# Kernel tuning notes

Hardware: AMD Instinct MI355X
Metric: run time of the kernel (lower is better)

## Reference

```python
import jax, jax.numpy as jnp
import numpy as np

C = 512
NUM_HEADS = 8
GROUPS = 32
EPS = 1e-5
SHAPE = (1, C, 4, 32, 32)  # B, C, T, H, W


def setup_inputs() -> dict:
    key = jax.random.key(0)
    k_x, k_qkv, k_proj = jax.random.split(key, 3)
    # Small init scale on weights keeps softmax logits in a sane range.
    return {
        "x": jax.random.normal(k_x, SHAPE, dtype=jnp.float32),
        "gn_w": jnp.ones((C,), dtype=jnp.float32),
        "gn_b": jnp.zeros((C,), dtype=jnp.float32),
        "qkv_w": jax.random.normal(k_qkv, (3 * C, C), dtype=jnp.float32) * 0.02,
        "qkv_b": jnp.zeros((3 * C,), dtype=jnp.float32),
        "proj_w": jax.random.normal(k_proj, (C, C), dtype=jnp.float32) * 0.02,
        "proj_b": jnp.zeros((C,), dtype=jnp.float32),
    }


def reference(x, gn_w, gn_b, qkv_w, qkv_b, proj_w, proj_b):
    B, Cc, T, H, W = x.shape
    N = T * H * W
    nh = NUM_HEADS
    hd = Cc // nh

    # GroupNorm(32, C)
    xg = x.reshape(B, GROUPS, -1)
    mean = jnp.mean(xg, axis=-1, keepdims=True)
    var = jnp.var(xg, axis=-1, keepdims=True)
    xn = ((xg - mean) * jax.lax.rsqrt(var + EPS)).reshape(B, Cc, N)
    xn = xn * gn_w[None, :, None] + gn_b[None, :, None]

    # 1x1x1 conv == channel GEMM
    qkv = jnp.einsum('oc,bcn->bon', qkv_w, xn) + qkv_b[None, :, None]
    qkv = qkv.reshape(B, 3, nh, hd, N)
    q, k, v = qkv[:, 0], qkv[:, 1], qkv[:, 2]  # [B, nh, hd, N]

    scale = hd ** (-0.5)
    attn = jnp.einsum('bhdt,bhds->bhts', q, k) * scale  # [B, nh, N, N]
    attn = jax.nn.softmax(attn, axis=-1)
    out = jnp.einsum('bhts,bhds->bhdt', attn, v)  # [B, nh, hd, N]
    out = out.reshape(B, Cc, N)

    out = jnp.einsum('oc,bcn->bon', proj_w, out) + proj_b[None, :, None]
    return out.reshape(B, Cc, T, H, W) + x
```

## Files before the change

### kernel.cpp

```cpp
#include <hip/hip_runtime.h>
#include <hip/hip_bf16.h>

#define SEQN 4096
#define HD 64
#define CCH 512
#define NH 8
#define SC 4
#define CHUNK (SEQN / SC)

typedef __attribute__((ext_vector_type(8))) short short8;
typedef __attribute__((ext_vector_type(4))) float f32x4;

#define AS1 __attribute__((address_space(1)))
#define AS3 __attribute__((address_space(3)))

#if __has_builtin(__builtin_amdgcn_exp2f)
#define EXP2(x) __builtin_amdgcn_exp2f(x)
#else
#define EXP2(x) exp2f(x)
#endif

#define QSCALE 0.18033688011112042f

static __device__ __forceinline__ unsigned short f2bf(float f) {
    __hip_bfloat16 h = __float2bfloat16(f);
    return *(unsigned short*)&h;
}
static __device__ __forceinline__ float bf2f(unsigned short u) {
    unsigned int v = ((unsigned int)u) << 16;
    return *(float*)&v;
}
static __device__ __forceinline__ unsigned int fbits(float f) { return *(unsigned int*)&f; }
static __device__ __forceinline__ float hi_f(unsigned int v) {
    unsigned int t = v & 0xFFFF0000u; return *(float*)&t;
}
static __device__ __forceinline__ float lo_f(unsigned int v) {
    unsigned int t = v << 16; return *(float*)&t;
}
static __device__ __forceinline__ unsigned int pkbf(float lo, float hi) {
    return (fbits(hi) & 0xFFFF0000u) | (fbits(lo) >> 16);
}
static __device__ __forceinline__ short8 half_frag(unsigned int a, unsigned int b) {
    uint4 u; u.x = a; u.y = b; u.z = 0u; u.w = 0u;
    return __builtin_bit_cast(short8, u);
}
static __device__ __forceinline__ void load_lds_16(const unsigned short* g, unsigned short* l) {
    __builtin_amdgcn_global_load_lds((const AS1 void*)g, (AS3 void*)l, 16, 0, 0);
}

__global__ __launch_bounds__(256) void gn_stats(const float* __restrict__ x,
                                                float2* __restrict__ partials) {
    const int b = blockIdx.x;
    const int g = b >> 3;
    const int slice = b & 7;
    const float* xs = x + (size_t)g * 65536 + slice * 8192;
    const int tid = threadIdx.x;
    float s = 0.f, ss = 0.f;
    for (int i = tid; i < 2048; i += 256) {
        float4 v = ((const float4*)xs)[i];
        s  += v.x + v.y + v.z + v.w;
        ss += v.x * v.x + v.y * v.y + v.z * v.z + v.w * v.w;
    }
    for (int off = 32; off; off >>= 1) {
        s  += __shfl_xor(s, off);
        ss += __shfl_xor(ss, off);
    }
    __shared__ float red[8];
    const int wave = tid >> 6;
    const int lane = tid & 63;
    if (lane == 0) { red[wave] = s; red[4 + wave] = ss; }
    __syncthreads();
    if (tid == 0) {
        partials[b] = make_float2(red[0] + red[1] + red[2] + red[3],
                                  red[4] + red[5] + red[6] + red[7]);
    }
}

__global__ __launch_bounds__(256) void gn_norm_t(const float* __restrict__ x,
                                                 const float2* __restrict__ partials,
                                                 const float* __restrict__ w,
                                                 const float* __restrict__ b,
                                                 unsigned short* __restrict__ xnT) {
    __shared__ float tile[64][65];
    __shared__ float gmean[4], grstd[4];
    const int t0 = blockIdx.x * 64;
    const int c0 = blockIdx.y * 64;
    const int tid = threadIdx.x;
    if (tid < 4) {
        int g = (c0 >> 4) + tid;
        float s = 0.f, ss = 0.f;
#pragma unroll
        for (int i = 0; i < 8; i++) {
            float2 p = partials[g * 8 + i];
            s += p.x; ss += p.y;
        }
        float mean = s * (1.f / 65536.f);
        float var  = ss * (1.f / 65536.f) - mean * mean;
        gmean[tid] = mean;
        grstd[tid] = rsqrtf(var + 1e-5f);
    }
    __syncthreads();
    for (int e = tid; e < 1024; e += 256) {
        int r  = e >> 4;
        int t4 = (e & 15) << 2;
        int c = c0 + r;
        float rstd = grstd[r >> 4];
        float sc = w[c] * rstd;
        float sh = b[c] - gmean[r >> 4] * sc;
        float4 v = *(const float4*)(x + (size_t)c * SEQN + t0 + t4);
        tile[r][t4 + 0] = v.x * sc + sh;
        tile[r][t4 + 1] = v.y * sc + sh;
        tile[r][t4 + 2] = v.z * sc + sh;
        tile[r][t4 + 3] = v.w * sc + sh;
    }
    __syncthreads();
    for (int e = tid; e < 1024; e += 256) {
        int t  = e >> 4;
        int c4 = (e & 15) << 2;
        ushort4 o;
        o.x = f2bf(tile[c4 + 0][t]);
        o.y = f2bf(tile[c4 + 1][t]);
        o.z = f2bf(tile[c4 + 2][t]);
        o.w = f2bf(tile[c4 + 3][t]);
        *(ushort4*)(xnT + (size_t)(t0 + t) * CCH + c0 + c4) = o;
    }
}

__global__ __launch_bounds__(256) void cvt_w(const float* __restrict__ qkv_w,
                                             const float* __restrict__ proj_w,
                                             unsigned short* __restrict__ wq,
                                             unsigned short* __restrict__ wp) {
    const int i = blockIdx.x * 256 + threadIdx.x;
    const int NQ = 3 * CCH * CCH / 4;
    float4 f;
    unsigned short* d;
    if (i < NQ) { f = ((const float4*)qkv_w)[i]; d = wq + (size_t)i * 4; }
    else        { f = ((const float4*)proj_w)[i - NQ]; d = wp + (size_t)(i - NQ) * 4; }
    ushort4 o;
    o.x = f2bf(f.x); o.y = f2bf(f.y); o.z = f2bf(f.z); o.w = f2bf(f.w);
    *(ushort4*)d = o;
}

__global__ __launch_bounds__(256) void gemm_qkv(const unsigned short* __restrict__ Wb,
                                                const unsigned short* __restrict__ xnT,
                                                const float* __restrict__ bias,
                                                unsigned short* __restrict__ qt,
                                                unsigned short* __restrict__ kt,
                                                unsigned short* __restrict__ vv) {
    __shared__ __align__(16) unsigned short Asm[128 * 64];
    __shared__ __align__(16) unsigned short Bsm[128 * 64];
    const int tid = threadIdx.x;
    const int wave = tid >> 6;
    const int lane = tid & 63;
    const int quad = lane >> 4;
    const int l15  = lane & 15;
    const int wm = wave >> 1, wn = wave & 1;
    const int nb = blockIdx.x, mb = blockIdx.y;
    const int sl = lane >> 3, slot = lane & 7;
    const int scol = (slot ^ sl) * 8;

    f32x4 acc[4][4];
#pragma unroll
    for (int mt = 0; mt < 4; mt++)
#pragma unroll
        for (int nt = 0; nt < 4; nt++) acc[mt][nt] = (f32x4){0.f, 0.f, 0.f, 0.f};

    for (int kb = 0; kb < CCH; kb += 64) {
        __syncthreads();
#pragma unroll
        for (int i = 0; i < 4; i++) {
            const int c = wave * 4 + i;
            const int row = c * 8 + sl;
            load_lds_16(Wb  + (size_t)(mb * 128 + row) * CCH + kb + scol, &Asm[c * 512]);
            load_lds_16(xnT + (size_t)(nb * 128 + row) * CCH + kb + scol, &Bsm[c * 512]);
        }
        __syncthreads();
#pragma unroll
        for (int kk = 0; kk < 2; kk++) {
            const int so = ((kk * 4 + quad) ^ (l15 & 7)) << 3;
            short8 a[4], b[4];
#pragma unroll
            for (int mt = 0; mt < 4; mt++)
                a[mt] = *(const short8*)(Asm + (wm * 64 + mt * 16 + l15) * 64 + so);
#pragma unroll
            for (int nt = 0; nt < 4; nt++)
                b[nt] = *(const short8*)(Bsm + (wn * 64 + nt * 16 + l15) * 64 + so);
#pragma unroll
            for (int mt = 0; mt < 4; mt++)
#pragma unroll
                for (int nt = 0; nt < 4; nt++)
                    acc[mt][nt] = __builtin_amdgcn_mfma_f32_16x16x32_bf16(a[mt], b[nt], acc[mt][nt], 0, 0, 0);
        }
    }

    const int sel = mb >> 2;
#pragma unroll
    for (int mt = 0; mt < 4; mt++) {
        const int m0 = mb * 128 + wm * 64 + mt * 16 + quad * 4;
        float bs[4] = {bias[m0], bias[m0 + 1], bias[m0 + 2], bias[m0 + 3]};
        if (sel < 2) {
            unsigned short* dst = sel ? kt : qt;
            const float mul = sel ? 1.0f : QSCALE;
            const int h  = (m0 >> 6) & 7;
            const int d0 = m0 & 63;
#pragma unroll
            for (int nt = 0; nt < 4; nt++) {
                const int t = nb * 128 + wn * 64 + nt * 16 + l15;
                ushort4 o;
                o.x = f2bf((acc[mt][nt][0] + bs[0]) * mul);
                o.y = f2bf((acc[mt][nt][1] + bs[1]) * mul);
                o.z = f2bf((acc[mt][nt][2] + bs[2]) * mul);
                o.w = f2bf((acc[mt][nt][3] + bs[3]) * mul);
                *(ushort4*)(dst + ((size_t)h * SEQN + t) * HD + d0) = o;
            }
        } else {
            const int c0 = m0 - 1024;
#pragma unroll
            for (int nt = 0; nt < 4; nt++) {
                const int t = nb * 128 + wn * 64 + nt * 16 + l15;
#pragma unroll
                for (int reg = 0; reg < 4; reg++)
                    vv[(size_t)(c0 + reg) * SEQN + t] = f2bf(acc[mt][nt][reg] + bs[reg]);
            }
        }
    }
}

__global__ __launch_bounds__(256) void gemm_proj(const unsigned short* __restrict__ Wb,
                                                 const unsigned short* __restrict__ attnoT,
                                                 const float* __restrict__ bias,
                                                 const float* __restrict__ resid,
                                                 float* __restrict__ out) {
    __shared__ __align__(16) unsigned short Asm[64 * 64];
    __shared__ __align__(16) unsigned short Bsm[128 * 64];
    const int tid = threadIdx.x;
    const int wave = tid >> 6;
    const int lane = tid & 63;
    const int quad = lane >> 4;
    const int l15  = lane & 15;
    const int wm = wave >> 1, wn = wave & 1;
    const int nb = blockIdx.x, mb = blockIdx.y;
    const int sl = lane >> 3, slot = lane & 7;
    const int scol = (slot ^ sl) * 8;

    f32x4 acc[2][4];
#pragma unroll
    for (int mt = 0; mt < 2; mt++)
#pragma unroll
        for (int nt = 0; nt < 4; nt++) acc[mt][nt] = (f32x4){0.f, 0.f, 0.f, 0.f};

    for (int kb = 0; kb < CCH; kb += 64) {
        __syncthreads();
#pragma unroll
        for (int i = 0; i < 2; i++) {
            const int c = wave * 2 + i;
            const int row = c * 8 + sl;
            load_lds_16(Wb + (size_t)(mb * 64 + row) * CCH + kb + scol, &Asm[c * 512]);
        }
#pragma unroll
        for (int i = 0; i < 4; i++) {
            const int c = wave * 4 + i;
            const int row = c * 8 + sl;
            load_lds_16(attnoT + (size_t)(nb * 128 + row) * CCH + kb + scol, &Bsm[c * 512]);
        }
        __syncthreads();
#pragma unroll
        for (int kk = 0; kk < 2; kk++) {
            const int so = ((kk * 4 + quad) ^ (l15 & 7)) << 3;
            short8 a[2], b[4];
#pragma unroll
            for (int mt = 0; mt < 2; mt++)
                a[mt] = *(const short8*)(Asm + (wm * 32 + mt * 16 + l15) * 64 + so);
#pragma unroll
            for (int nt = 0; nt < 4; nt++)
                b[nt] = *(const short8*)(Bsm + (wn * 64 + nt * 16 + l15) * 64 + so);
#pragma unroll
            for (int mt = 0; mt < 2; mt++)
#pragma unroll
                for (int nt = 0; nt < 4; nt++)
                    acc[mt][nt] = __builtin_amdgcn_mfma_f32_16x16x32_bf16(a[mt], b[nt], acc[mt][nt], 0, 0, 0);
        }
    }

#pragma unroll
    for (int mt = 0; mt < 2; mt++) {
        const int m0 = mb * 64 + wm * 32 + mt * 16 + quad * 4;
        float bs[4] = {bias[m0], bias[m0 + 1], bias[m0 + 2], bias[m0 + 3]};
#pragma unroll
        for (int nt = 0; nt < 4; nt++) {
            const int n = nb * 128 + wn * 64 + nt * 16 + l15;
#pragma unroll
            for (int reg = 0; reg < 4; reg++) {
                const size_t off = (size_t)(m0 + reg) * SEQN + n;
                out[off] = acc[mt][nt][reg] + bs[reg] + resid[off];
            }
        }
    }
}

__global__ __launch_bounds__(256) void attn(const unsigned short* __restrict__ qt,
                                            const unsigned short* __restrict__ kt,
                                            const unsigned short* __restrict__ vv,
                                            unsigned short* __restrict__ po,
                                            float2* __restrict__ ml) {
    const int tid  = threadIdx.x;
    const int wave = tid >> 6;
    const int lane = tid & 63;
    const int quad = lane >> 4;
    const int l15  = lane & 15;
    const int ws = wave >> 1;
    const int wt = wave & 1;
    const int h  = blockIdx.z;
    const int cb = blockIdx.y;
    const int tb = blockIdx.x * 64;

    const unsigned short* qh = qt + (size_t)h * SEQN * HD;
    const unsigned short* kh = kt + (size_t)h * SEQN * HD;
    const unsigned short* vh = vv + (size_t)h * HD * SEQN;

    __shared__ __align__(16) unsigned short kv[2][8192];
    __shared__ float lredm[4][2][16];

    const int sl = lane >> 3, slot = lane & 7;
    const int scol = (slot ^ sl) * 8;

    short8 qf[2][2];
#pragma unroll
    for (int nt = 0; nt < 2; nt++) {
        const unsigned short* qp = qh + (size_t)(tb + wt * 32 + nt * 16 + l15) * HD + quad * 8;
        qf[nt][0] = *(const short8*)(qp);
        qf[nt][1] = *(const short8*)(qp + 32);
    }

    f32x4 oacc[4][2];
#pragma unroll
    for (int dt = 0; dt < 4; dt++)
#pragma unroll
        for (int nt = 0; nt < 2; nt++) oacc[dt][nt] = (f32x4){0.f, 0.f, 0.f, 0.f};
    float lsum[2] = {0.f, 0.f};

    const int s_beg = cb * CHUNK;
    const int NIT = CHUNK / 64;

    auto stage = [&](int buf, int s0) {
#pragma unroll
        for (int i = 0; i < 2; i++) {
            const int c = wave * 2 + i;
            const int row = c * 8 + sl;
            load_lds_16(kh + (size_t)(s0 + row) * HD + scol, &kv[buf][c * 512]);
            load_lds_16(vh + (size_t)row * SEQN + s0 + scol, &kv[buf][4096 + c * 512]);
        }
    };

    stage(0, s_beg);

    for (int it = 0; it < NIT; it++) {
        const int cur = it & 1;
        __syncthreads();
        if (it + 1 < NIT) stage(cur ^ 1, s_beg + (it + 1) * 64);

        const unsigned short* ks  = kv[cur];
        const unsigned short* vsb = kv[cur] + 4096;

        short8 ka[2][2];
#pragma unroll
        for (int sm = 0; sm < 2; sm++) {
            const unsigned short* kp = ks + (ws * 32 + sm * 16 + l15) * 64;
            ka[sm][0] = *(const short8*)(kp + (((quad    ) ^ (l15 & 7)) << 3));
            ka[sm][1] = *(const short8*)(kp + (((quad + 4) ^ (l15 & 7)) << 3));
        }
        f32x4 sacc[2][2];
#pragma unroll
        for (int sm = 0; sm < 2; sm++)
#pragma unroll
            for (int nt = 0; nt < 2; nt++) {
                f32x4 z = (f32x4){0.f, 0.f, 0.f, 0.f};
                z = __builtin_amdgcn_mfma_f32_16x16x32_bf16(ka[sm][0], qf[nt][0], z, 0, 0, 0);
                sacc[sm][nt] = __builtin_amdgcn_mfma_f32_16x16x32_bf16(ka[sm][1], qf[nt][1], z, 0, 0, 0);
            }

        unsigned int pbw[2][2][2];
#pragma unroll
        for (int sm = 0; sm < 2; sm++)
#pragma unroll
            for (int nt = 0; nt < 2; nt++) {
                float p0 = EXP2(sacc[sm][nt][0]);
                float p1 = EXP2(sacc[sm][nt][1]);
                float p2 = EXP2(sacc[sm][nt][2]);
                float p3 = EXP2(sacc[sm][nt][3]);
                lsum[nt] += (p0 + p1) + (p2 + p3);
                pbw[sm][nt][0] = pkbf(p0, p1);
                pbw[sm][nt][1] = pkbf(p2, p3);
            }

#pragma unroll
        for (int dt = 0; dt < 4; dt++) {
            const int row = dt * 16 + l15;
#pragma unroll
            for (int sm = 0; sm < 2; sm++) {
                const int col8 = ws * 4 + sm * 2 + (quad >> 1);
                const unsigned short* vp = vsb + row * 64 +
                    ((col8 ^ (l15 & 7)) << 3) + ((quad & 1) << 2);
                uint2 vd = *(const uint2*)vp;
                short8 va = half_frag(vd.x, vd.y);
#pragma unroll
                for (int nt = 0; nt < 2; nt++)
                    oacc[dt][nt] = __builtin_amdgcn_mfma_f32_16x16x32_bf16(
                        va, half_frag(pbw[sm][nt][0], pbw[sm][nt][1]), oacc[dt][nt], 0, 0, 0);
            }
        }
    }

    __syncthreads();
    unsigned int* exg = (unsigned int*)&kv[0][0];
#pragma unroll
    for (int nt = 0; nt < 2; nt++) {
        lsum[nt] += __shfl_xor(lsum[nt], 16);
        lsum[nt] += __shfl_xor(lsum[nt], 32);
    }
    if (quad == 0) {
        lredm[wave][0][l15] = lsum[0];
        lredm[wave][1][l15] = lsum[1];
    }
#pragma unroll
    for (int j = 0; j < 2; j++) {
        const int dt = (ws ^ 1) * 2 + j;
#pragma unroll
        for (int nt = 0; nt < 2; nt++) {
            const int idx = (((wave * 2 + j) * 2 + nt) * 64 + lane) * 2;
            exg[idx]     = pkbf(oacc[dt][nt][0], oacc[dt][nt][1]);
            exg[idx + 1] = pkbf(oacc[dt][nt][2], oacc[dt][nt][3]);
        }
    }
    __syncthreads();
    const int pw = wave ^ 2;
    float lt[2];
#pragma unroll
    for (int nt = 0; nt < 2; nt++)
        lt[nt] = lredm[wave][nt][l15] + lredm[pw][nt][l15];

#pragma unroll
    for (int j = 0; j < 2; j++) {
        const int dtm = ws * 2 + j;
#pragma unroll
        for (int nt = 0; nt < 2; nt++) {
            const int idx = (((pw * 2 + j) * 2 + nt) * 64 + lane) * 2;
            unsigned int r0 = exg[idx], r1 = exg[idx + 1];
            f32x4 o = oacc[dtm][nt];
            o[0] += lo_f(r0); o[1] += hi_f(r0);
            o[2] += lo_f(r1); o[3] += hi_f(r1);
            const float rl = 1.0f / lt[nt];
            const int t = tb + wt * 32 + nt * 16 + l15;
            ushort4 ov;
            ov.x = f2bf(o[0] * rl); ov.y = f2bf(o[1] * rl);
            ov.z = f2bf(o[2] * rl); ov.w = f2bf(o[3] * rl);
            *(ushort4*)(po + ((size_t)(cb * NH + h) * SEQN + t) * HD + dtm * 16 + quad * 4) = ov;
            if (ws == 0 && quad == 0 && j == 0)
                ml[(size_t)(cb * NH + h) * SEQN + t] = make_float2(0.f, lt[nt]);
        }
    }
}

__global__ __launch_bounds__(256) void attn_merge(const unsigned short* __restrict__ po,
                                                  const float2* __restrict__ ml,
                                                  unsigned short* __restrict__ attnoT) {
    const int idx = blockIdx.x * 256 + threadIdx.x;
    const int t  = idx >> 7;
    const int c4 = (idx & 127) << 2;
    const int h  = c4 >> 6;
    const int d  = c4 & 63;

    float a0 = 0.f, a1 = 0.f, a2 = 0.f, a3 = 0.f, denom = 0.f;
#pragma unroll
    for (int cb = 0; cb < SC; cb++) {
        float wgt = ml[(size_t)(cb * NH + h) * SEQN + t].y;
        denom += wgt;
        ushort4 o = *(const ushort4*)(po + ((size_t)(cb * NH + h) * SEQN + t) * HD + d);
        a0 += wgt * bf2f(o.x);
        a1 += wgt * bf2f(o.y);
        a2 += wgt * bf2f(o.z);
        a3 += wgt * bf2f(o.w);
    }
    const float rd = 1.0f / denom;
    ushort4 r;
    r.x = f2bf(a0 * rd); r.y = f2bf(a1 * rd); r.z = f2bf(a2 * rd); r.w = f2bf(a3 * rd);
    *(ushort4*)(attnoT + (size_t)t * CCH + c4) = r;
}

extern "C" void kernel_launch(void* const* d_in, const int* in_sizes, int n_in,
                              void* d_out, int out_size, void* d_ws, size_t ws_size,
                              hipStream_t stream) {
    const float* x      = (const float*)d_in[0];
    const float* gn_w   = (const float*)d_in[1];
    const float* gn_b   = (const float*)d_in[2];
    const float* qkv_w  = (const float*)d_in[3];
    const float* qkv_b  = (const float*)d_in[4];
    const float* proj_w = (const float*)d_in[5];
    const float* proj_b = (const float*)d_in[6];
    float* out = (float*)d_out;

    char* ws = (char*)d_ws;
    float2* partials = (float2*)ws;
    unsigned short* xnT   = (unsigned short*)(ws + 2048);
    unsigned short* wq_bf = xnT + (size_t)SEQN * CCH;
    unsigned short* wp_bf = wq_bf + (size_t)3 * CCH * CCH;
    unsigned short* qt    = wp_bf + (size_t)CCH * CCH;
    unsigned short* kt    = qt + (size_t)NH * SEQN * HD;
    unsigned short* vv    = kt + (size_t)NH * SEQN * HD;
    unsigned short* po    = vv + (size_t)NH * SEQN * HD;
    unsigned short* attnoT = po + (size_t)SC * NH * SEQN * HD;
    float2* ml = (float2*)(attnoT + (size_t)SEQN * CCH);

    gn_stats<<<256, 256, 0, stream>>>(x, partials);
    gn_norm_t<<<dim3(SEQN / 64, CCH / 64), 256, 0, stream>>>(x, partials, gn_w, gn_b, xnT);
    cvt_w<<<(3 * CCH * CCH + CCH * CCH) / 4 / 256, 256, 0, stream>>>(qkv_w, proj_w, wq_bf, wp_bf);
    gemm_qkv<<<dim3(SEQN / 128, 3 * CCH / 128), 256, 0, stream>>>(wq_bf, xnT, qkv_b, qt, kt, vv);
    attn<<<dim3(SEQN / 64, SC, NH), 256, 0, stream>>>(qt, kt, vv, po, ml);
    attn_merge<<<SEQN * 128 / 256, 256, 0, stream>>>(po, ml, attnoT);
    gemm_proj<<<dim3(SEQN / 128, CCH / 64), 256, 0, stream>>>(wp_bf, attnoT, proj_b, x, out);
}
```

Baseline: 197.0 us.

## Enlarge attention query tile, shrink QKV GEMM M tile, fuse prep kernels

The attention kernel now handles 128 queries per block instead of 64. Each wave covers 64 query columns, so every K/V tile staged in LDS is reused across twice as many queries. The K/V loop is unrolled by two with explicit ping-pong buffers and precomputed LDS offsets, and exp and pack are fused right after the score MFMA. Separately, the QKV GEMM M tile is halved to 64 so more blocks fill the device, and the GN stats and weight conversion kernels are merged into one launch. The larger attention tile raises register pressure (launch bounds hint set to 2 blocks per SM) and halves the attention grid size.

```diff
diff --git a/kernel.cpp b/kernel.cpp
--- a/kernel.cpp
+++ b/kernel.cpp
@@ -7,6 +7,7 @@
 #define NH 8
 #define SC 4
 #define CHUNK (SEQN / SC)
+#define TBK 128
 
 typedef __attribute__((ext_vector_type(8))) short short8;
 typedef __attribute__((ext_vector_type(4))) float f32x4;
@@ -48,31 +49,46 @@
     __builtin_amdgcn_global_load_lds((const AS1 void*)g, (AS3 void*)l, 16, 0, 0);
 }
 
-__global__ __launch_bounds__(256) void gn_stats(const float* __restrict__ x,
-                                                float2* __restrict__ partials) {
-    const int b = blockIdx.x;
-    const int g = b >> 3;
-    const int slice = b & 7;
-    const float* xs = x + (size_t)g * 65536 + slice * 8192;
+__global__ __launch_bounds__(256) void prep(const float* __restrict__ x,
+                                            float2* __restrict__ partials,
+                                            const float* __restrict__ qkv_w,
+                                            const float* __restrict__ proj_w,
+                                            unsigned short* __restrict__ wq,
+                                            unsigned short* __restrict__ wp) {
     const int tid = threadIdx.x;
-    float s = 0.f, ss = 0.f;
-    for (int i = tid; i < 2048; i += 256) {
-        float4 v = ((const float4*)xs)[i];
-        s  += v.x + v.y + v.z + v.w;
-        ss += v.x * v.x + v.y * v.y + v.z * v.z + v.w * v.w;
-    }
-    for (int off = 32; off; off >>= 1) {
-        s  += __shfl_xor(s, off);
-        ss += __shfl_xor(ss, off);
-    }
-    __shared__ float red[8];
-    const int wave = tid >> 6;
-    const int lane = tid & 63;
-    if (lane == 0) { red[wave] = s; red[4 + wave] = ss; }
-    __syncthreads();
-    if (tid == 0) {
-        partials[b] = make_float2(red[0] + red[1] + red[2] + red[3],
-                                  red[4] + red[5] + red[6] + red[7]);
+    if (blockIdx.x < 256) {
+        const int b = blockIdx.x;
+        const int g = b >> 3;
+        const int slice = b & 7;
+        const float* xs = x + (size_t)g * 65536 + slice * 8192;
+        float s = 0.f, ss = 0.f;
+        for (int i = tid; i < 2048; i += 256) {
+            float4 v = ((const float4*)xs)[i];
+            s  += v.x + v.y + v.z + v.w;
+            ss += v.x * v.x + v.y * v.y + v.z * v.z + v.w * v.w;
+        }
+        for (int off = 32; off; off >>= 1) {
+            s  += __shfl_xor(s, off);
+            ss += __shfl_xor(ss, off);
+        }
+        __shared__ float red[8];
+        const int wave = tid >> 6;
+        const int lane = tid & 63;
+        if (lane == 0) { red[wave] = s; red[4 + wave] = ss; }
+        __syncthreads();
+        if (tid == 0)
+            partials[b] = make_float2(red[0] + red[1] + red[2] + red[3],
+                                      red[4] + red[5] + red[6] + red[7]);
+    } else {
+        const int i = (blockIdx.x - 256) * 256 + tid;
+        const int NQ = 3 * CCH * CCH / 4;
+        float4 f;
+        unsigned short* d;
+        if (i < NQ) { f = ((const float4*)qkv_w)[i]; d = wq + (size_t)i * 4; }
+        else        { f = ((const float4*)proj_w)[i - NQ]; d = wp + (size_t)(i - NQ) * 4; }
+        ushort4 o;
+        o.x = f2bf(f.x); o.y = f2bf(f.y); o.z = f2bf(f.z); o.w = f2bf(f.w);
+        *(ushort4*)d = o;
     }
 }
 
@@ -126,28 +142,13 @@
     }
 }
 
-__global__ __launch_bounds__(256) void cvt_w(const float* __restrict__ qkv_w,
-                                             const float* __restrict__ proj_w,
-                                             unsigned short* __restrict__ wq,
-                                             unsigned short* __restrict__ wp) {
-    const int i = blockIdx.x * 256 + threadIdx.x;
-    const int NQ = 3 * CCH * CCH / 4;
-    float4 f;
-    unsigned short* d;
-    if (i < NQ) { f = ((const float4*)qkv_w)[i]; d = wq + (size_t)i * 4; }
-    else        { f = ((const float4*)proj_w)[i - NQ]; d = wp + (size_t)(i - NQ) * 4; }
-    ushort4 o;
-    o.x = f2bf(f.x); o.y = f2bf(f.y); o.z = f2bf(f.z); o.w = f2bf(f.w);
-    *(ushort4*)d = o;
-}
-
 __global__ __launch_bounds__(256) void gemm_qkv(const unsigned short* __restrict__ Wb,
                                                 const unsigned short* __restrict__ xnT,
                                                 const float* __restrict__ bias,
                                                 unsigned short* __restrict__ qt,
                                                 unsigned short* __restrict__ kt,
                                                 unsigned short* __restrict__ vv) {
-    __shared__ __align__(16) unsigned short Asm[128 * 64];
+    __shared__ __align__(16) unsigned short Asm[64 * 64];
     __shared__ __align__(16) unsigned short Bsm[128 * 64];
     const int tid = threadIdx.x;
     const int wave = tid >> 6;
@@ -159,44 +160,49 @@
     const int sl = lane >> 3, slot = lane & 7;
     const int scol = (slot ^ sl) * 8;
 
-    f32x4 acc[4][4];
-#pragma unroll
-    for (int mt = 0; mt < 4; mt++)
+    f32x4 acc[2][4];
+#pragma unroll
+    for (int mt = 0; mt < 2; mt++)
 #pragma unroll
         for (int nt = 0; nt < 4; nt++) acc[mt][nt] = (f32x4){0.f, 0.f, 0.f, 0.f};
 
     for (int kb = 0; kb < CCH; kb += 64) {
         __syncthreads();
+#pragma unroll
+        for (int i = 0; i < 2; i++) {
+            const int c = wave * 2 + i;
+            const int row = c * 8 + sl;
+            load_lds_16(Wb + (size_t)(mb * 64 + row) * CCH + kb + scol, &Asm[c * 512]);
+        }
 #pragma unroll
         for (int i = 0; i < 4; i++) {
             const int c = wave * 4 + i;
             const int row = c * 8 + sl;
-            load_lds_16(Wb  + (size_t)(mb * 128 + row) * CCH + kb + scol, &Asm[c * 512]);
             load_lds_16(xnT + (size_t)(nb * 128 + row) * CCH + kb + scol, &Bsm[c * 512]);
         }
         __syncthreads();
 #pragma unroll
         for (int kk = 0; kk < 2; kk++) {
             const int so = ((kk * 4 + quad) ^ (l15 & 7)) << 3;
-            short8 a[4], b[4];
-#pragma unroll
-            for (int mt = 0; mt < 4; mt++)
-                a[mt] = *(const short8*)(Asm + (wm * 64 + mt * 16 + l15) * 64 + so);
+            short8 a[2], b[4];
+#pragma unroll
+            for (int mt = 0; mt < 2; mt++)
+                a[mt] = *(const short8*)(Asm + (wm * 32 + mt * 16 + l15) * 64 + so);
 #pragma unroll
             for (int nt = 0; nt < 4; nt++)
                 b[nt] = *(const short8*)(Bsm + (wn * 64 + nt * 16 + l15) * 64 + so);
 #pragma unroll
-            for (int mt = 0; mt < 4; mt++)
+            for (int mt = 0; mt < 2; mt++)
 #pragma unroll
                 for (int nt = 0; nt < 4; nt++)
                     acc[mt][nt] = __builtin_amdgcn_mfma_f32_16x16x32_bf16(a[mt], b[nt], acc[mt][nt], 0, 0, 0);
         }
     }
 
-    const int sel = mb >> 2;
-#pragma unroll
-    for (int mt = 0; mt < 4; mt++) {
-        const int m0 = mb * 128 + wm * 64 + mt * 16 + quad * 4;
+    const int sel = mb >> 3;
+#pragma unroll
+    for (int mt = 0; mt < 2; mt++) {
+        const int m0 = mb * 64 + wm * 32 + mt * 16 + quad * 4;
         float bs[4] = {bias[m0], bias[m0 + 1], bias[m0 + 2], bias[m0 + 3]};
         if (sel < 2) {
             unsigned short* dst = sel ? kt : qt;
@@ -298,11 +304,11 @@
     }
 }
 
-__global__ __launch_bounds__(256) void attn(const unsigned short* __restrict__ qt,
-                                            const unsigned short* __restrict__ kt,
-                                            const unsigned short* __restrict__ vv,
-                                            unsigned short* __restrict__ po,
-                                            float2* __restrict__ ml) {
+__global__ __launch_bounds__(256, 2) void attn(const unsigned short* __restrict__ qt,
+                                               const unsigned short* __restrict__ kt,
+                                               const unsigned short* __restrict__ vv,
+                                               unsigned short* __restrict__ po,
+                                               float2* __restrict__ ml) {
     const int tid  = threadIdx.x;
     const int wave = tid >> 6;
     const int lane = tid & 63;
@@ -312,151 +318,156 @@
     const int wt = wave & 1;
     const int h  = blockIdx.z;
     const int cb = blockIdx.y;
-    const int tb = blockIdx.x * 64;
+    const int tb = blockIdx.x * TBK;
 
     const unsigned short* qh = qt + (size_t)h * SEQN * HD;
     const unsigned short* kh = kt + (size_t)h * SEQN * HD;
     const unsigned short* vh = vv + (size_t)h * HD * SEQN;
 
     __shared__ __align__(16) unsigned short kv[2][8192];
-    __shared__ float lredm[4][2][16];
+    __shared__ float lredm[4][4][16];
 
     const int sl = lane >> 3, slot = lane & 7;
     const int scol = (slot ^ sl) * 8;
-
-    short8 qf[2][2];
-#pragma unroll
-    for (int nt = 0; nt < 2; nt++) {
-        const unsigned short* qp = qh + (size_t)(tb + wt * 32 + nt * 16 + l15) * HD + quad * 8;
+    const int x7 = l15 & 7;
+
+    int kaoff[2][2];
+#pragma unroll
+    for (int sm = 0; sm < 2; sm++)
+#pragma unroll
+        for (int k = 0; k < 2; k++)
+            kaoff[sm][k] = (ws * 32 + sm * 16 + l15) * 64 + (((k * 4 + quad) ^ x7) << 3);
+    int vpoff[4][2];
+#pragma unroll
+    for (int dt = 0; dt < 4; dt++)
+#pragma unroll
+        for (int sm = 0; sm < 2; sm++)
+            vpoff[dt][sm] = 4096 + (dt * 16 + l15) * 64 +
+                            (((ws * 4 + sm * 2 + (quad >> 1)) ^ x7) << 3) + ((quad & 1) << 2);
+
+    short8 qf[4][2];
+#pragma unroll
+    for (int nt = 0; nt < 4; nt++) {
+        const unsigned short* qp = qh + (size_t)(tb + wt * 64 + nt * 16 + l15) * HD + quad * 8;
         qf[nt][0] = *(const short8*)(qp);
         qf[nt][1] = *(const short8*)(qp + 32);
     }
 
-    f32x4 oacc[4][2];
+    f32x4 oacc[4][4];
 #pragma unroll
     for (int dt = 0; dt < 4; dt++)
 #pragma unroll
-        for (int nt = 0; nt < 2; nt++) oacc[dt][nt] = (f32x4){0.f, 0.f, 0.f, 0.f};
-    float lsum[2] = {0.f, 0.f};
+        for (int nt = 0; nt < 4; nt++) oacc[dt][nt] = (f32x4){0.f, 0.f, 0.f, 0.f};
+    float lsum[4] = {0.f, 0.f, 0.f, 0.f};
 
     const int s_beg = cb * CHUNK;
     const int NIT = CHUNK / 64;
 
-    auto stage = [&](int buf, int s0) {
-#pragma unroll
-        for (int i = 0; i < 2; i++) {
-            const int c = wave * 2 + i;
-            const int row = c * 8 + sl;
-            load_lds_16(kh + (size_t)(s0 + row) * HD + scol, &kv[buf][c * 512]);
-            load_lds_16(vh + (size_t)row * SEQN + s0 + scol, &kv[buf][4096 + c * 512]);
-        }
-    };
-
-    stage(0, s_beg);
-
-    for (int it = 0; it < NIT; it++) {
-        const int cur = it & 1;
-        __syncthreads();
-        if (it + 1 < NIT) stage(cur ^ 1, s_beg + (it + 1) * 64);
-
-        const unsigned short* ks  = kv[cur];
-        const unsigned short* vsb = kv[cur] + 4096;
-
+    const unsigned short* kgp  = kh + (size_t)(s_beg + wave * 16 + sl) * HD + scol;
+    const unsigned short* vgp0 = vh + (size_t)(wave * 16 + sl) * SEQN + s_beg + scol;
+    const unsigned short* vgp1 = vgp0 + (size_t)8 * SEQN;
+
+    load_lds_16(kgp,          &kv[0][(wave * 2 + 0) * 512]);
+    load_lds_16(kgp + 8 * HD, &kv[0][(wave * 2 + 1) * 512]);
+    load_lds_16(vgp0, &kv[0][4096 + (wave * 2 + 0) * 512]);
+    load_lds_16(vgp1, &kv[0][4096 + (wave * 2 + 1) * 512]);
+    kgp += 64 * HD; vgp0 += 64; vgp1 += 64;
+
+    auto compute = [&](const unsigned short* ksb) {
         short8 ka[2][2];
 #pragma unroll
         for (int sm = 0; sm < 2; sm++) {
-            const unsigned short* kp = ks + (ws * 32 + sm * 16 + l15) * 64;
-            ka[sm][0] = *(const short8*)(kp + (((quad    ) ^ (l15 & 7)) << 3));
-            ka[sm][1] = *(const short8*)(kp + (((quad + 4) ^ (l15 & 7)) << 3));
-        }
-        f32x4 sacc[2][2];
+            ka[sm][0] = *(const short8*)(ksb + kaoff[sm][0]);
+            ka[sm][1] = *(const short8*)(ksb + kaoff[sm][1]);
+        }
+        short8 pfrag[2][4];
 #pragma unroll
         for (int sm = 0; sm < 2; sm++)
 #pragma unroll
-            for (int nt = 0; nt < 2; nt++) {
+            for (int nt = 0; nt < 4; nt++) {
                 f32x4 z = (f32x4){0.f, 0.f, 0.f, 0.f};
                 z = __builtin_amdgcn_mfma_f32_16x16x32_bf16(ka[sm][0], qf[nt][0], z, 0, 0, 0);
-                sacc[sm][nt] = __builtin_amdgcn_mfma_f32_16x16x32_bf16(ka[sm][1], qf[nt][1], z, 0, 0, 0);
+                z = __builtin_amdgcn_mfma_f32_16x16x32_bf16(ka[sm][1], qf[nt][1], z, 0, 0, 0);
+                float p0 = EXP2(z[0]);
+                float p1 = EXP2(z[1]);
+                float p2 = EXP2(z[2]);
+                float p3 = EXP2(z[3]);
+                lsum[nt] += (p0 + p1) + (p2 + p3);
+                pfrag[sm][nt] = half_frag(pkbf(p0, p1), pkbf(p2, p3));
             }
-
-        unsigned int pbw[2][2][2];
-#pragma unroll
-        for (int sm = 0; sm < 2; sm++)
-#pragma unroll
-            for (int nt = 0; nt < 2; nt++) {
-                float p0 = EXP2(sacc[sm][nt][0]);
-                float p1 = EXP2(sacc[sm][nt][1]);
-                float p2 = EXP2(sacc[sm][nt][2]);
-                float p3 = EXP2(sacc[sm][nt][3]);
-                lsum[nt] += (p0 + p1) + (p2 + p3);
-                pbw[sm][nt][0] = pkbf(p0, p1);
-                pbw[sm][nt][1] = pkbf(p2, p3);
+#pragma unroll
+        for (int dt = 0; dt < 4; dt++)
+#pragma unroll
+            for (int sm = 0; sm < 2; sm++) {
+                uint2 vd = *(const uint2*)(ksb + vpoff[dt][sm]);
+                short8 va = half_frag(vd.x, vd.y);
+#pragma unroll
+                for (int nt = 0; nt < 4; nt++)
+                    oacc[dt][nt] = __builtin_amdgcn_mfma_f32_16x16x32_bf16(va, pfrag[sm][nt], oacc[dt][nt], 0, 0, 0);
             }
-
-#pragma unroll
-        for (int dt = 0; dt < 4; dt++) {
-            const int row = dt * 16 + l15;
-#pragma unroll
-            for (int sm = 0; sm < 2; sm++) {
-                const int col8 = ws * 4 + sm * 2 + (quad >> 1);
-                const unsigned short* vp = vsb + row * 64 +
-                    ((col8 ^ (l15 & 7)) << 3) + ((quad & 1) << 2);
-                uint2 vd = *(const uint2*)vp;
-                short8 va = half_frag(vd.x, vd.y);
-#pragma unroll
-                for (int nt = 0; nt < 2; nt++)
-                    oacc[dt][nt] = __builtin_amdgcn_mfma_f32_16x16x32_bf16(
-                        va, half_frag(pbw[sm][nt][0], pbw[sm][nt][1]), oacc[dt][nt], 0, 0, 0);
-            }
-        }
+    };
+
+    for (int it2 = 0; it2 < NIT / 2; it2++) {
+        __syncthreads();
+        load_lds_16(kgp,          &kv[1][(wave * 2 + 0) * 512]);
+        load_lds_16(kgp + 8 * HD, &kv[1][(wave * 2 + 1) * 512]);
+        load_lds_16(vgp0, &kv[1][4096 + (wave * 2 + 0) * 512]);
+        load_lds_16(vgp1, &kv[1][4096 + (wave * 2 + 1) * 512]);
+        kgp += 64 * HD; vgp0 += 64; vgp1 += 64;
+        compute(&kv[0][0]);
+        __syncthreads();
+        if (it2 + 1 < NIT / 2) {
+            load_lds_16(kgp,          &kv[0][(wave * 2 + 0) * 512]);
+            load_lds_16(kgp + 8 * HD, &kv[0][(wave * 2 + 1) * 512]);
+            load_lds_16(vgp0, &kv[0][4096 + (wave * 2 + 0) * 512]);
+            load_lds_16(vgp1, &kv[0][4096 + (wave * 2 + 1) * 512]);
+            kgp += 64 * HD; vgp0 += 64; vgp1 += 64;
+        }
+        compute(&kv[1][0]);
     }
 
     __syncthreads();
     unsigned int* exg = (unsigned int*)&kv[0][0];
 #pragma unroll
-    for (int nt = 0; nt < 2; nt++) {
+    for (int nt = 0; nt < 4; nt++) {
         lsum[nt] += __shfl_xor(lsum[nt], 16);
         lsum[nt] += __shfl_xor(lsum[nt], 32);
     }
     if (quad == 0) {
-        lredm[wave][0][l15] = lsum[0];
-        lredm[wave][1][l15] = lsum[1];
+#pragma unroll
+        for (int nt = 0; nt < 4; nt++) lredm[wave][nt][l15] = lsum[nt];
     }
 #pragma unroll
     for (int j = 0; j < 2; j++) {
         const int dt = (ws ^ 1) * 2 + j;
 #pragma unroll
-        for (int nt = 0; nt < 2; nt++) {
-            const int idx = (((wave * 2 + j) * 2 + nt) * 64 + lane) * 2;
+        for (int nt = 0; nt < 4; nt++) {
+            const int idx = (((wave * 2 + j) * 4 + nt) * 64 + lane) * 2;
             exg[idx]     = pkbf(oacc[dt][nt][0], oacc[dt][nt][1]);
             exg[idx + 1] = pkbf(oacc[dt][nt][2], oacc[dt][nt][3]);
         }
     }
     __syncthreads();
     const int pw = wave ^ 2;
-    float lt[2];
-#pragma unroll
-    for (int nt = 0; nt < 2; nt++)
-        lt[nt] = lredm[wave][nt][l15] + lredm[pw][nt][l15];
-
 #pragma unroll
     for (int j = 0; j < 2; j++) {
         const int dtm = ws * 2 + j;
 #pragma unroll
-        for (int nt = 0; nt < 2; nt++) {
-            const int idx = (((pw * 2 + j) * 2 + nt) * 64 + lane) * 2;
+        for (int nt = 0; nt < 4; nt++) {
+            const float lt = lredm[wave][nt][l15] + lredm[pw][nt][l15];
+            const int idx = (((pw * 2 + j) * 4 + nt) * 64 + lane) * 2;
             unsigned int r0 = exg[idx], r1 = exg[idx + 1];
             f32x4 o = oacc[dtm][nt];
             o[0] += lo_f(r0); o[1] += hi_f(r0);
             o[2] += lo_f(r1); o[3] += hi_f(r1);
-            const float rl = 1.0f / lt[nt];
-            const int t = tb + wt * 32 + nt * 16 + l15;
+            const float rl = 1.0f / lt;
+            const int t = tb + wt * 64 + nt * 16 + l15;
             ushort4 ov;
             ov.x = f2bf(o[0] * rl); ov.y = f2bf(o[1] * rl);
             ov.z = f2bf(o[2] * rl); ov.w = f2bf(o[3] * rl);
             *(ushort4*)(po + ((size_t)(cb * NH + h) * SEQN + t) * HD + dtm * 16 + quad * 4) = ov;
             if (ws == 0 && quad == 0 && j == 0)
-                ml[(size_t)(cb * NH + h) * SEQN + t] = make_float2(0.f, lt[nt]);
+                ml[(size_t)(cb * NH + h) * SEQN + t] = make_float2(0.f, lt);
         }
     }
 }
@@ -511,11 +522,11 @@
     unsigned short* attnoT = po + (size_t)SC * NH * SEQN * HD;
     float2* ml = (float2*)(attnoT + (size_t)SEQN * CCH);
 
-    gn_stats<<<256, 256, 0, stream>>>(x, partials);
+    prep<<<256 + (3 * CCH * CCH + CCH * CCH) / 4 / 256, 256, 0, stream>>>(
+        x, partials, qkv_w, proj_w, wq_bf, wp_bf);
     gn_norm_t<<<dim3(SEQN / 64, CCH / 64), 256, 0, stream>>>(x, partials, gn_w, gn_b, xnT);
-    cvt_w<<<(3 * CCH * CCH + CCH * CCH) / 4 / 256, 256, 0, stream>>>(qkv_w, proj_w, wq_bf, wp_bf);
-    gemm_qkv<<<dim3(SEQN / 128, 3 * CCH / 128), 256, 0, stream>>>(wq_bf, xnT, qkv_b, qt, kt, vv);
-    attn<<<dim3(SEQN / 64, SC, NH), 256, 0, stream>>>(qt, kt, vv, po, ml);
+    gemm_qkv<<<dim3(SEQN / 128, 3 * CCH / 64), 256, 0, stream>>>(wq_bf, xnT, qkv_b, qt, kt, vv);
+    attn<<<dim3(SEQN / TBK, SC, NH), 256, 0, stream>>>(qt, kt, vv, po, ml);
     attn_merge<<<SEQN * 128 / 256, 256, 0, stream>>>(po, ml, attnoT);
     gemm_proj<<<dim3(SEQN / 128, CCH / 64), 256, 0, stream>>>(wp_bf, attnoT, proj_b, x, out);
 }
```

After: 278.7 us. 41.5% more time.
